# Kernel optimization log

Measured on AMD Instinct MI355X. Metric: run time of the kernel, lower is better.

The kernel has to match this reference:

```python
import jax, jax.numpy as jnp
import numpy as np


def setup_inputs() -> dict:
    key = jax.random.key(0)
    ks = jax.random.split(key, 9)
    B, C, H, W = 8, 256, 64, 64
    Co = 256
    s = 1.0 / np.sqrt(C)
    return {
        "x": jax.random.normal(ks[0], (B, C, H, W), dtype=jnp.float32),
        "wq": jax.random.normal(ks[1], (Co, C), dtype=jnp.float32) * s,
        "bq": jnp.zeros((Co,), dtype=jnp.float32),
        "wk": jax.random.normal(ks[2], (Co, C), dtype=jnp.float32) * s,
        "bk": jnp.zeros((Co,), dtype=jnp.float32),
        "wv": jax.random.normal(ks[3], (Co, C), dtype=jnp.float32) * s,
        "bv": jnp.zeros((Co,), dtype=jnp.float32),
        "wo": jax.random.normal(ks[4], (C, Co), dtype=jnp.float32) * s,
        "bo": jnp.zeros((C,), dtype=jnp.float32),
    }


def reference(x, wq, bq, wk, bk, wv, bv, wo, bo):
    B, C, H, W = x.shape
    # 1x1 conv == per-pixel matmul. Flatten spatial dims: [B, N, C], N = H*W
    xf = x.reshape(B, C, H * W).transpose(0, 2, 1)  # [B, N, C]
    q = jnp.einsum("bnc,oc->bno", xf, wq) + bq      # [B, N, Co]
    k = jnp.einsum("bnc,oc->bno", xf, wk) + bk      # [B, N, Co]
    v = jnp.einsum("bnc,oc->bno", xf, wv) + bv      # [B, N, Co]
    # attention[b, i, j] = q[b, i] . k[b, j]  (no scaling, matches source)
    attn = jax.nn.softmax(jnp.einsum("bio,bjo->bij", q, k), axis=-1)  # [B, N, N]
    # out[b, i, c] = sum_j attn[b, i, j] * v[b, j, c]
    out = jnp.einsum("bij,bjo->bio", attn, v)       # [B, N, Co]
    out = jnp.einsum("bno,co->bnc", out, wo) + bo   # [B, N, C]
    return out.transpose(0, 2, 1).reshape(B, C, H, W)
```

## Files before the change

kernel.cpp:

```cpp
#include <hip/hip_runtime.h>
#include <hip/hip_fp16.h>

typedef _Float16 f16;
typedef _Float16 f16x4 __attribute__((ext_vector_type(4)));
typedef _Float16 f16x8 __attribute__((ext_vector_type(8)));
typedef float f32x4 __attribute__((ext_vector_type(4)));
typedef float f32x16 __attribute__((ext_vector_type(16)));
typedef unsigned int u32;
typedef u32 u32x4 __attribute__((ext_vector_type(4)));

static constexpr int CB = 8;
static constexpr int CC = 256;
static constexpr int CN = 4096;

#define MFMA(a, b, c)   __builtin_amdgcn_mfma_f32_16x16x32_f16((a), (b), (c), 0, 0, 0)
#define MFMA32(a, b, c) __builtin_amdgcn_mfma_f32_32x32x16_f16((a), (b), (c), 0, 0, 0)

__device__ __forceinline__ void gll16(const void* g, void* l) {
  __builtin_amdgcn_global_load_lds(
      (const __attribute__((address_space(1))) unsigned int*)g,
      (__attribute__((address_space(3))) unsigned int*)l, 16, 0, 0);
}

__device__ __forceinline__ void plswap(u32& a, u32& b) {
  asm volatile("v_permlane32_swap_b32 %0, %1" : "+v"(a), "+v"(b));
}

__device__ __forceinline__ u32 pk(float lo, float hi) {
  auto h = __builtin_amdgcn_cvt_pkrtz(lo, hi);
  return __builtin_bit_cast(u32, h);
}

__global__ __launch_bounds__(256) void prep_weights(const float* __restrict__ wq,
    const float* __restrict__ wk, const float* __restrict__ wv,
    const float* __restrict__ wo, f16* __restrict__ W) {
  int i = blockIdx.x * 256 + threadIdx.x;
  W[i]          = (f16)wq[i];
  W[65536 + i]  = (f16)wk[i];
  W[131072 + i] = (f16)wv[i];
  W[196608 + i] = (f16)wo[i];
}

__global__ __launch_bounds__(256) void qkv_kernel(const float* __restrict__ x,
    const f16* __restrict__ Wq, const f16* __restrict__ Wk, const f16* __restrict__ Wv,
    const float* __restrict__ bq, const float* __restrict__ bk, const float* __restrict__ bv,
    f16* __restrict__ Q, f16* __restrict__ K, f16* __restrict__ Vt) {
  __shared__ f16 xf[64][264];
  const int b  = blockIdx.x >> 6;
  const int n0 = (blockIdx.x & 63) << 6;
  const int t  = threadIdx.x;
  const float* xb = x + (size_t)b * CC * CN;
  {
    int c = t >> 4;
    const int nn = (t & 15) << 2;
    #pragma unroll
    for (int pass = 0; pass < 16; ++pass, c += 16) {
      const float4 v = *(const float4*)(xb + (size_t)c * CN + n0 + nn);
      xf[nn + 0][c] = (f16)v.x;
      xf[nn + 1][c] = (f16)v.y;
      xf[nn + 2][c] = (f16)v.z;
      xf[nn + 3][c] = (f16)v.w;
    }
  }
  __syncthreads();
  const int w = t >> 6, l = t & 63, lr = l & 15, lh = l >> 4;

  f16x8 xff[8];
  #pragma unroll
  for (int kk = 0; kk < 8; ++kk)
    xff[kk] = *(const f16x8*)&xf[w * 16 + lr][kk * 32 + lh * 8];

  const size_t qkrow = ((size_t)b * CN + n0 + w * 16 + lr) * CC;

  #pragma unroll 1
  for (int mat = 0; mat < 2; ++mat) {
    const f16* W = mat ? Wk : Wq;
    const float* bias = mat ? bk : bq;
    f16* dst = mat ? K : Q;
    f32x4 acc[16];
    #pragma unroll
    for (int m = 0; m < 16; ++m) acc[m] = f32x4{0.f, 0.f, 0.f, 0.f};
    #pragma unroll
    for (int kk = 0; kk < 8; ++kk) {
      #pragma unroll
      for (int m = 0; m < 16; ++m) {
        f16x8 af = *(const f16x8*)&W[(size_t)(m * 16 + lr) * CC + kk * 32 + lh * 8];
        acc[m] = MFMA(af, xff[kk], acc[m]);
      }
    }
    #pragma unroll
    for (int m = 0; m < 16; ++m) {
      const int o = m * 16 + lh * 4;
      const float4 bs = *(const float4*)&bias[o];
      f16x4 hv;
      hv[0] = (f16)(acc[m][0] + bs.x);
      hv[1] = (f16)(acc[m][1] + bs.y);
      hv[2] = (f16)(acc[m][2] + bs.z);
      hv[3] = (f16)(acc[m][3] + bs.w);
      *(f16x4*)&dst[qkrow + o] = hv;
    }
  }
  {
    f32x4 acc[16];
    #pragma unroll
    for (int m = 0; m < 16; ++m) acc[m] = f32x4{0.f, 0.f, 0.f, 0.f};
    #pragma unroll
    for (int kk = 0; kk < 8; ++kk) {
      #pragma unroll
      for (int m = 0; m < 16; ++m) {
        f16x8 bf = *(const f16x8*)&Wv[(size_t)(m * 16 + lr) * CC + kk * 32 + lh * 8];
        acc[m] = MFMA(xff[kk], bf, acc[m]);
      }
    }
    #pragma unroll
    for (int m = 0; m < 16; ++m) {
      const int o = m * 16 + lr;
      const float bvs = bv[o];
      f16x4 hv;
      #pragma unroll
      for (int j = 0; j < 4; ++j) hv[j] = (f16)(acc[m][j] + bvs);
      *(f16x4*)&Vt[((size_t)b * CC + o) * CN + n0 + w * 16 + lh * 4] = hv;
    }
  }
}

__global__ __launch_bounds__(256, 2) void attn_kernel(const f16* __restrict__ Q,
    const f16* __restrict__ K, const f16* __restrict__ Vt, f16* __restrict__ O) {
  __shared__ __align__(16) char SMEM[75264];

  const int bid = blockIdx.x;
  const int lb = ((bid & 7) << 6) | (bid >> 3);
  const int b  = lb >> 6;
  const int q0 = (lb & 63) << 6;
  const int tid = threadIdx.x;
  const int w  = tid >> 6, l = tid & 63, ln = l & 31, lh = l >> 5;
  const int g  = w >> 1, hv = w & 1;

  const f16* Qb = Q  + (size_t)b * CN * CC;
  const f16* Kb = K  + (size_t)b * CN * CC;
  const f16* Vb = Vt + (size_t)b * CC * CN;

  auto kfrm = [&](int buf, int ks) -> char* { return SMEM + (buf << 14) + (ks << 10); };
  auto vfrm = [&](int buf, int f)  -> char* { return SMEM + 32768 + (buf << 14) + (f << 10); };
  auto pfrm = [&](int pb, int fr)  -> char* { return SMEM + 65536 + (pb << 12) + (g << 11) + (fr << 10); };
  float* const MLm = (float*)(SMEM + 73728 + g * 256);
  float* const MLl = MLm + 32;
  auto AFa = [&](int pb) -> float* { return (float*)(SMEM + 74240 + (pb << 9) + (g << 8)); };

  auto stageK = [&](int buf, int kv0) {
    const f16* ksrc = Kb + (size_t)(kv0 + ln) * CC + (w * 4) * 16 + 8 * lh;
    #pragma unroll
    for (int j = 0; j < 4; ++j)
      gll16(ksrc + j * 16, kfrm(buf, w * 4 + j));
  };
  auto stageV = [&](int buf, int kv0) {
    #pragma unroll
    for (int p = 0; p < 2; ++p) {
      const int f = w * 4 + 2 * p;
      const f16* vsrc = Vb + (size_t)((f >> 1) * 32 + ln) * CN + kv0 + 8 * lh;
      gll16(vsrc,      vfrm(buf, f));
      gll16(vsrc + 16, vfrm(buf, f + 1));
    }
  };

  const int qrow = q0 + 32 * g + ln;
  f16x8 qf[16];
  #pragma unroll
  for (int ks = 0; ks < 16; ++ks)
    qf[ks] = *(const f16x8*)(Qb + (size_t)qrow * CC + ks * 16 + 8 * lh);

  f32x16 oacc[4];
  #pragma unroll
  for (int ot = 0; ot < 4; ++ot)
    #pragma unroll
    for (int i = 0; i < 16; ++i) oacc[ot][i] = 0.0f;

  auto pvstep = [&](int pb) {
    const float* af = AFa(pb);
    const float flag = af[32];
    if (flag != 0.0f) {
      #pragma unroll
      for (int r = 0; r < 16; ++r) {
        const float fr = af[(r & 3) + 8 * (r >> 2) + 4 * lh];
        #pragma unroll
        for (int ot = 0; ot < 4; ++ot) oacc[ot][r] *= fr;
      }
    }
    const f16x8 pa0 = *(const f16x8*)(pfrm(pb, 0) + l * 16);
    const f16x8 pa1 = *(const f16x8*)(pfrm(pb, 1) + l * 16);
    __builtin_amdgcn_s_setprio(1);
    #pragma unroll
    for (int ot = 0; ot < 4; ++ot) {
      const int f0 = 8 * hv + 2 * ot;
      const f16x8 v0 = *(const f16x8*)(vfrm(pb, f0) + l * 16);
      oacc[ot] = MFMA32(pa0, v0, oacc[ot]);
      const f16x8 v1 = *(const f16x8*)(vfrm(pb, f0 + 1) + l * 16);
      oacc[ot] = MFMA32(pa1, v1, oacc[ot]);
    }
    __builtin_amdgcn_s_setprio(0);
  };

  stageK(0, 0);
  __syncthreads();

  #pragma unroll 1
  for (int it = 0; it < 128; ++it) {
    const int cur = it & 1, prv = cur ^ 1;
    if (it < 127) stageK(prv, (it + 1) * 32);
    stageV(cur, it * 32);

    const bool own = (hv == cur);

    f32x16 s;
    if (own) {
      #pragma unroll
      for (int i = 0; i < 16; ++i) s[i] = 0.0f;
      __builtin_amdgcn_s_setprio(1);
      #pragma unroll
      for (int ks = 0; ks < 16; ++ks) {
        const f16x8 kf = *(const f16x8*)(kfrm(cur, ks) + l * 16);
        s = MFMA32(kf, qf[ks], s);
      }
      __builtin_amdgcn_s_setprio(0);
    }

    if (it > 0) pvstep(prv);

    if (own) {
      const float mprev = it ? MLm[ln] : -3e38f;
      const float lprev = it ? MLl[ln] : 0.0f;
      float mx8[8], mx4[4];
      #pragma unroll
      for (int i = 0; i < 8; ++i) mx8[i] = fmaxf(s[2 * i], s[2 * i + 1]);
      #pragma unroll
      for (int i = 0; i < 4; ++i) mx4[i] = fmaxf(mx8[2 * i], mx8[2 * i + 1]);
      float pmax = fmaxf(fmaxf(mx4[0], mx4[1]), fmaxf(mx4[2], mx4[3]));
      pmax = fmaxf(pmax, __shfl_xor(pmax, 32));
      const bool need = !__all(pmax - mprev <= 8.0f);
      const float mnew = need ? fmaxf(mprev, pmax) : mprev;
      float p[16];
      #pragma unroll
      for (int r = 0; r < 16; ++r) p[r] = __expf(s[r] - mnew);
      float sm8[8], sm4[4];
      #pragma unroll
      for (int i = 0; i < 8; ++i) sm8[i] = p[2 * i] + p[2 * i + 1];
      #pragma unroll
      for (int i = 0; i < 4; ++i) sm4[i] = sm8[2 * i] + sm8[2 * i + 1];
      float psum = (sm4[0] + sm4[1]) + (sm4[2] + sm4[3]);
      psum += __shfl_xor(psum, 32);
      float alpha = 1.0f, lnew;
      if (need) { alpha = __expf(mprev - mnew); lnew = lprev * alpha + psum; }
      else      { lnew = lprev + psum; }
      if (l < 32) {
        MLm[ln] = mnew;
        MLl[ln] = lnew;
        float* af = AFa(cur);
        af[ln] = alpha;
        if (ln == 0) af[32] = need ? 1.0f : 0.0f;
      }
      u32 pw[8];
      #pragma unroll
      for (int i = 0; i < 8; ++i) pw[i] = pk(p[2 * i], p[2 * i + 1]);
      plswap(pw[0], pw[2]); plswap(pw[1], pw[3]);
      plswap(pw[4], pw[6]); plswap(pw[5], pw[7]);
      *(u32x4*)(pfrm(cur, 0) + l * 16) = u32x4{pw[0], pw[1], pw[2], pw[3]};
      *(u32x4*)(pfrm(cur, 1) + l * 16) = u32x4{pw[4], pw[5], pw[6], pw[7]};
    }
    __syncthreads();
  }

  pvstep(1);

  f16* Ob = O + ((size_t)b * CN + q0 + 32 * g) * CC + 128 * hv;
  #pragma unroll
  for (int r = 0; r < 16; ++r) {
    const int q = (r & 3) + 8 * (r >> 2) + 4 * lh;
    const float inv = 1.0f / MLl[q];
    #pragma unroll
    for (int ot = 0; ot < 4; ++ot)
      Ob[(size_t)q * CC + ot * 32 + ln] = (f16)(oacc[ot][r] * inv);
  }
}

__global__ __launch_bounds__(256) void oproj_kernel(const f16* __restrict__ O,
    const f16* __restrict__ Wo, const float* __restrict__ bo, float* __restrict__ out) {
  const int b  = blockIdx.x >> 6;
  const int n0 = (blockIdx.x & 63) << 6;
  const int t  = threadIdx.x;
  const int w = t >> 6, l = t & 63, lr = l & 15, lh = l >> 4;
  const f16* orow = O + ((size_t)b * CN + n0 + w * 16 + lr) * CC;
  f32x4 acc[16];
  #pragma unroll
  for (int m = 0; m < 16; ++m) acc[m] = f32x4{0.f, 0.f, 0.f, 0.f};
  #pragma unroll
  for (int kk = 0; kk < 8; ++kk) {
    const f16x8 bf = *(const f16x8*)&orow[kk * 32 + lh * 8];
    #pragma unroll
    for (int m = 0; m < 16; ++m) {
      f16x8 af = *(const f16x8*)&Wo[(size_t)(m * 16 + lr) * CC + kk * 32 + lh * 8];
      acc[m] = MFMA(af, bf, acc[m]);
    }
  }
  #pragma unroll
  for (int m = 0; m < 16; ++m) {
    const int c = m * 16 + lh * 4;
    const float4 bv4 = *(const float4*)&bo[c];
    const size_t base = ((size_t)b * CC + c) * CN + n0 + w * 16 + lr;
    out[base + 0 * (size_t)CN] = acc[m][0] + bv4.x;
    out[base + 1 * (size_t)CN] = acc[m][1] + bv4.y;
    out[base + 2 * (size_t)CN] = acc[m][2] + bv4.z;
    out[base + 3 * (size_t)CN] = acc[m][3] + bv4.w;
  }
}

extern "C" void kernel_launch(void* const* d_in, const int* in_sizes, int n_in,
                              void* d_out, int out_size, void* d_ws, size_t ws_size,
                              hipStream_t stream) {
  const float* x  = (const float*)d_in[0];
  const float* wq = (const float*)d_in[1];
  const float* bq = (const float*)d_in[2];
  const float* wk = (const float*)d_in[3];
  const float* bk = (const float*)d_in[4];
  const float* wv = (const float*)d_in[5];
  const float* bv = (const float*)d_in[6];
  const float* wo = (const float*)d_in[7];
  const float* bo = (const float*)d_in[8];

  f16* W  = (f16*)d_ws;
  f16* Qd = W + 262144;
  f16* Kd = Qd + (size_t)CB * CN * CC;
  f16* Vt = Kd + (size_t)CB * CN * CC;
  f16* Od = Vt + (size_t)CB * CN * CC;

  prep_weights<<<256, 256, 0, stream>>>(wq, wk, wv, wo, W);
  qkv_kernel<<<512, 256, 0, stream>>>(x, W, W + 65536, W + 131072, bq, bk, bv, Qd, Kd, Vt);
  attn_kernel<<<512, 256, 0, stream>>>(Qd, Kd, Vt, Od);
  oproj_kernel<<<512, 256, 0, stream>>>(Od, W + 196608, bo, (float*)d_out);
}
```

Before: 390.8 us.

## Fuse output projection into attention epilogue and split QK accumulation chains

Drops the separate oproj kernel: the attention kernel writes the normalized output tile to shared memory and immediately runs the Wo projection, storing fp32 results with bias directly. This removes the global round trip of the fp16 O tensor and one kernel launch. QK^T now uses two independent MFMA accumulators to shorten the dependency chain. Blocks alternate which wave half owns the softmax step by parity, to balance the two SIMD halves across co-resident blocks. The fused epilogue adds register and shared memory pressure at the end of the attention kernel.

```diff
diff --git a/kernel.cpp b/kernel.cpp
--- a/kernel.cpp
+++ b/kernel.cpp
@@ -125,13 +125,16 @@
 }
 
 __global__ __launch_bounds__(256, 2) void attn_kernel(const f16* __restrict__ Q,
-    const f16* __restrict__ K, const f16* __restrict__ Vt, f16* __restrict__ O) {
+    const f16* __restrict__ K, const f16* __restrict__ Vt,
+    const f16* __restrict__ Wo, const float* __restrict__ bo,
+    float* __restrict__ out) {
   __shared__ __align__(16) char SMEM[75264];
 
   const int bid = blockIdx.x;
   const int lb = ((bid & 7) << 6) | (bid >> 3);
   const int b  = lb >> 6;
   const int q0 = (lb & 63) << 6;
+  const int par = (bid >> 3) & 1;
   const int tid = threadIdx.x;
   const int w  = tid >> 6, l = tid & 63, ln = l & 31, lh = l >> 5;
   const int g  = w >> 1, hv = w & 1;
@@ -209,19 +212,24 @@
     if (it < 127) stageK(prv, (it + 1) * 32);
     stageV(cur, it * 32);
 
-    const bool own = (hv == cur);
+    const bool own = (hv == ((it + par) & 1));
 
     f32x16 s;
     if (own) {
-      #pragma unroll
-      for (int i = 0; i < 16; ++i) s[i] = 0.0f;
+      f32x16 sa, sb;
+      #pragma unroll
+      for (int i = 0; i < 16; ++i) { sa[i] = 0.0f; sb[i] = 0.0f; }
       __builtin_amdgcn_s_setprio(1);
       #pragma unroll
-      for (int ks = 0; ks < 16; ++ks) {
-        const f16x8 kf = *(const f16x8*)(kfrm(cur, ks) + l * 16);
-        s = MFMA32(kf, qf[ks], s);
+      for (int ks = 0; ks < 8; ++ks) {
+        const f16x8 kf0 = *(const f16x8*)(kfrm(cur, ks) + l * 16);
+        sa = MFMA32(kf0, qf[ks], sa);
+        const f16x8 kf1 = *(const f16x8*)(kfrm(cur, ks + 8) + l * 16);
+        sb = MFMA32(kf1, qf[ks + 8], sb);
       }
       __builtin_amdgcn_s_setprio(0);
+      #pragma unroll
+      for (int i = 0; i < 16; ++i) s[i] = sa[i] + sb[i];
     }
 
     if (it > 0) pvstep(prv);
@@ -270,46 +278,48 @@
   }
 
   pvstep(1);
-
-  f16* Ob = O + ((size_t)b * CN + q0 + 32 * g) * CC + 128 * hv;
+  float invv[16];
+  #pragma unroll
+  for (int r = 0; r < 16; ++r)
+    invv[r] = 1.0f / MLl[(r & 3) + 8 * (r >> 2) + 4 * lh];
+  __syncthreads();
+
+  f16* const OT = (f16*)SMEM;
   #pragma unroll
   for (int r = 0; r < 16; ++r) {
     const int q = (r & 3) + 8 * (r >> 2) + 4 * lh;
-    const float inv = 1.0f / MLl[q];
+    const int qq = 32 * g + q;
     #pragma unroll
     for (int ot = 0; ot < 4; ++ot)
-      Ob[(size_t)q * CC + ot * 32 + ln] = (f16)(oacc[ot][r] * inv);
-  }
-}
-
-__global__ __launch_bounds__(256) void oproj_kernel(const f16* __restrict__ O,
-    const f16* __restrict__ Wo, const float* __restrict__ bo, float* __restrict__ out) {
-  const int b  = blockIdx.x >> 6;
-  const int n0 = (blockIdx.x & 63) << 6;
-  const int t  = threadIdx.x;
-  const int w = t >> 6, l = t & 63, lr = l & 15, lh = l >> 4;
-  const f16* orow = O + ((size_t)b * CN + n0 + w * 16 + lr) * CC;
-  f32x4 acc[16];
-  #pragma unroll
-  for (int m = 0; m < 16; ++m) acc[m] = f32x4{0.f, 0.f, 0.f, 0.f};
-  #pragma unroll
-  for (int kk = 0; kk < 8; ++kk) {
-    const f16x8 bf = *(const f16x8*)&orow[kk * 32 + lh * 8];
+      OT[qq * 264 + 128 * hv + ot * 32 + ln] = (f16)(oacc[ot][r] * invv[r]);
+  }
+  __syncthreads();
+
+  {
+    const int lr = l & 15, lq = l >> 4;
+    const f16* orow = OT + (w * 16 + lr) * 264;
+    f32x4 acc[16];
+    #pragma unroll
+    for (int m = 0; m < 16; ++m) acc[m] = f32x4{0.f, 0.f, 0.f, 0.f};
+    #pragma unroll
+    for (int kk = 0; kk < 8; ++kk) {
+      const f16x8 bf = *(const f16x8*)&orow[kk * 32 + lq * 8];
+      #pragma unroll
+      for (int m = 0; m < 16; ++m) {
+        f16x8 af = *(const f16x8*)&Wo[(size_t)(m * 16 + lr) * CC + kk * 32 + lq * 8];
+        acc[m] = MFMA(af, bf, acc[m]);
+      }
+    }
     #pragma unroll
     for (int m = 0; m < 16; ++m) {
-      f16x8 af = *(const f16x8*)&Wo[(size_t)(m * 16 + lr) * CC + kk * 32 + lh * 8];
-      acc[m] = MFMA(af, bf, acc[m]);
-    }
-  }
-  #pragma unroll
-  for (int m = 0; m < 16; ++m) {
-    const int c = m * 16 + lh * 4;
-    const float4 bv4 = *(const float4*)&bo[c];
-    const size_t base = ((size_t)b * CC + c) * CN + n0 + w * 16 + lr;
-    out[base + 0 * (size_t)CN] = acc[m][0] + bv4.x;
-    out[base + 1 * (size_t)CN] = acc[m][1] + bv4.y;
-    out[base + 2 * (size_t)CN] = acc[m][2] + bv4.z;
-    out[base + 3 * (size_t)CN] = acc[m][3] + bv4.w;
+      const int c = m * 16 + lq * 4;
+      const float4 bv4 = *(const float4*)&bo[c];
+      const size_t base = ((size_t)b * CC + c) * CN + q0 + w * 16 + lr;
+      out[base + 0 * (size_t)CN] = acc[m][0] + bv4.x;
+      out[base + 1 * (size_t)CN] = acc[m][1] + bv4.y;
+      out[base + 2 * (size_t)CN] = acc[m][2] + bv4.z;
+      out[base + 3 * (size_t)CN] = acc[m][3] + bv4.w;
+    }
   }
 }
 
@@ -330,10 +340,8 @@
   f16* Qd = W + 262144;
   f16* Kd = Qd + (size_t)CB * CN * CC;
   f16* Vt = Kd + (size_t)CB * CN * CC;
-  f16* Od = Vt + (size_t)CB * CN * CC;
 
   prep_weights<<<256, 256, 0, stream>>>(wq, wk, wv, wo, W);
   qkv_kernel<<<512, 256, 0, stream>>>(x, W, W + 65536, W + 131072, bq, bk, bv, Qd, Kd, Vt);
-  attn_kernel<<<512, 256, 0, stream>>>(Qd, Kd, Vt, Od);
-  oproj_kernel<<<512, 256, 0, stream>>>(Od, W + 196608, bo, (float*)d_out);
-}
+  attn_kernel<<<512, 256, 0, stream>>>(Qd, Kd, Vt, W + 196608, bo, (float*)d_out);
+}
```

After: 378.2 us. -3.2%, faster.
